# Performance work log

Measured on AMD Instinct MI355X. Metric: run time of the kernel, lower is better.

## Reference

```python
import jax, jax.numpy as jnp
import numpy as np

L, B, D_DEC, D_ALIGN, D_ENC = 2048, 64, 1024, 512, 1024


def setup_inputs() -> dict:
    key = jax.random.key(0)
    ks = jax.random.split(key, 8)
    s_tm1 = jax.random.normal(ks[0], (B, D_DEC), dtype=jnp.float32)
    xs_h = jax.random.normal(ks[1], (L, B, D_ENC), dtype=jnp.float32)
    uh = jax.random.normal(ks[2], (L, B, D_ALIGN), dtype=jnp.float32)
    # binary padding mask over source positions; guarantee >=1 valid position per column
    xs_mask = (jax.random.uniform(ks[3], (L, B)) > 0.1).astype(jnp.float32)
    xs_mask = xs_mask.at[0].set(1.0)
    sa_w = jax.random.normal(ks[4], (D_ALIGN, D_DEC), dtype=jnp.float32) / np.sqrt(D_DEC)
    sa_b = jnp.zeros((D_ALIGN,), dtype=jnp.float32)
    a1_w = jax.random.normal(ks[5], (1, D_ALIGN), dtype=jnp.float32) / np.sqrt(D_ALIGN)
    a1_b = jnp.zeros((1,), dtype=jnp.float32)
    return {"s_tm1": s_tm1, "xs_h": xs_h, "uh": uh, "xs_mask": xs_mask,
            "sa_w": sa_w, "sa_b": sa_b, "a1_w": a1_w, "a1_b": a1_b}


def reference(s_tm1, xs_h, uh, xs_mask, sa_w, sa_b, a1_w, a1_b):
    # sa(s_tm1): (B, A)
    proj = s_tm1 @ sa_w.T + sa_b
    # broadcast add over source positions, tanh: (L, B, A)
    act = jnp.tanh(proj[None, :, :] + uh)
    # a1(...).squeeze(2): (L, B)
    score = jnp.einsum('lba,a->lb', act, a1_w[0]) + a1_b[0]
    # masked softmax over dim 0 (exp * mask, then normalize) as in MaskSoftmax
    e = jnp.exp(score - jnp.max(score, axis=0, keepdims=True)) * xs_mask
    e_ij = e / jnp.sum(e, axis=0, keepdims=True)
    # weighted sum of encoder states: (B, D_ENC)
    attend = jnp.einsum('lb,lbd->bd', e_ij, xs_h)
    return (e_ij, attend)
```

## Files before the change

kernel.cpp:

```cpp
#include <hip/hip_runtime.h>

#define L 2048
#define B 64
#define D_DEC 1024
#define D_ALIGN 512
#define D_ENC 1024
#define LSPLIT 32

using u32 = unsigned int;
using u16 = unsigned short;

__device__ __forceinline__ u16 f2bf(float f) {
    u32 u = __float_as_uint(f);
    u32 r = (u + 0x7fffu + ((u >> 16) & 1u)) >> 16;
    return (u16)r;
}
__device__ __forceinline__ float tanh_fast(float x) {
    float t = __expf(2.0f * x);
    return 1.0f - 2.0f * __builtin_amdgcn_rcpf(t + 1.0f);
}
__device__ __forceinline__ bool detect_bf(const void* xs_mask) {
    return ((const u32*)xs_mask)[0] == 0x3F803F80u;
}
__device__ __forceinline__ float ldv(const void* p, size_t i, bool bf) {
    if (bf) return __uint_as_float(((u32)((const u16*)p)[i]) << 16);
    return ((const float*)p)[i];
}

__global__ __launch_bounds__(256) void proj_kernel(const void* __restrict__ s_tm1,
                                                   const void* __restrict__ sa_w,
                                                   const void* __restrict__ c0,
                                                   const void* __restrict__ c1,
                                                   const void* __restrict__ xs_mask,
                                                   float* __restrict__ proj) {
    bool bf = detect_bf(xs_mask);
    u32 w0 = ((const u32*)c0)[0], w1 = ((const u32*)c1)[0];
    const void* sab = (w0 == 0u || w1 != 0u) ? c0 : c1;
    int b = blockIdx.x >> 3;
    int wid = threadIdx.x >> 6, lane = threadIdx.x & 63;
    int a0 = (blockIdx.x & 7) * 64 + wid * 16;
    size_t sb = (size_t)b * D_DEC + (size_t)lane * 16;
    float sreg[16];
    if (!bf) {
        const float4* s4 = (const float4*)((const float*)s_tm1 + sb);
#pragma unroll
        for (int m = 0; m < 4; ++m) {
            float4 v = s4[m];
            sreg[4*m] = v.x; sreg[4*m+1] = v.y; sreg[4*m+2] = v.z; sreg[4*m+3] = v.w;
        }
    } else {
#pragma unroll
        for (int m = 0; m < 16; ++m) sreg[m] = ldv(s_tm1, sb + m, bf);
    }
#pragma unroll 4
    for (int ai = 0; ai < 16; ++ai) {
        int a = a0 + ai;
        size_t wb = (size_t)a * D_DEC + (size_t)lane * 16;
        float acc = 0.f;
        if (!bf) {
            const float4* w4 = (const float4*)((const float*)sa_w + wb);
#pragma unroll
            for (int m = 0; m < 4; ++m) {
                float4 v = w4[m];
                acc += sreg[4*m] * v.x + sreg[4*m+1] * v.y
                     + sreg[4*m+2] * v.z + sreg[4*m+3] * v.w;
            }
        } else {
#pragma unroll
            for (int m = 0; m < 16; ++m) acc += sreg[m] * ldv(sa_w, wb + m, bf);
        }
#pragma unroll
        for (int off = 32; off; off >>= 1) acc += __shfl_xor(acc, off, 64);
        if (lane == 0) proj[b * D_ALIGN + a] = acc + ldv(sab, a, bf);
    }
}

__global__ __launch_bounds__(256) void score_kernel(const void* __restrict__ uh,
                                                    const void* __restrict__ c0,
                                                    const void* __restrict__ c1,
                                                    const void* __restrict__ a1_b,
                                                    const void* __restrict__ xs_mask,
                                                    const float* __restrict__ proj,
                                                    float* __restrict__ score_t) {
    bool bf = detect_bf(xs_mask);
    u32 w0 = ((const u32*)c0)[0], w1 = ((const u32*)c1)[0];
    const void* a1w = (w1 != 0u || w0 == 0u) ? c1 : c0;
    int wave = blockIdx.x * 4 + (threadIdx.x >> 6);
    int lane = threadIdx.x & 63;
    int b = wave & (B - 1);
    int lc = wave >> 6;
    float bias = ldv(a1_b, 0, bf);
    float s[8];
    if (!bf) {
        const float4* p4 = (const float4*)proj + (size_t)b * 128;
        const float4* w4 = (const float4*)a1w;
        float4 p[2], w[2];
#pragma unroll
        for (int j = 0; j < 2; ++j) { p[j] = p4[j * 64 + lane]; w[j] = w4[j * 64 + lane]; }
#pragma unroll
        for (int il = 0; il < 8; ++il) {
            int l = lc * 8 + il;
            const float4* u4 = (const float4*)uh + (size_t)(l * B + b) * 128;
            float v = 0.f;
#pragma unroll
            for (int j = 0; j < 2; ++j) {
                float4 u = u4[j * 64 + lane];
                v += tanh_fast(p[j].x + u.x) * w[j].x;
                v += tanh_fast(p[j].y + u.y) * w[j].y;
                v += tanh_fast(p[j].z + u.z) * w[j].z;
                v += tanh_fast(p[j].w + u.w) * w[j].w;
            }
            s[il] = v;
        }
    } else {
        float p[8], w[8];
#pragma unroll
        for (int j = 0; j < 8; ++j) {
            p[j] = proj[b * D_ALIGN + j * 64 + lane];
            w[j] = ldv(a1w, j * 64 + lane, bf);
        }
#pragma unroll
        for (int il = 0; il < 8; ++il) {
            int l = lc * 8 + il;
            size_t base = (size_t)(l * B + b) * D_ALIGN;
            float v = 0.f;
#pragma unroll
            for (int j = 0; j < 8; ++j)
                v += tanh_fast(p[j] + ldv(uh, base + j * 64 + lane, bf)) * w[j];
            s[il] = v;
        }
    }
#pragma unroll
    for (int il = 0; il < 8; ++il) {
        float v = s[il];
#pragma unroll
        for (int off = 32; off; off >>= 1) v += __shfl_xor(v, off, 64);
        s[il] = v;
    }
    if (lane == 0) {
#pragma unroll
        for (int il = 0; il < 8; ++il)
            score_t[(size_t)b * L + lc * 8 + il] = s[il] + bias;
    }
}

__global__ __launch_bounds__(256) void softmax_kernel(const void* __restrict__ xs_mask,
                                                      const float* __restrict__ score_t,
                                                      float* __restrict__ e_t,
                                                      void* __restrict__ out) {
    bool bf = detect_bf(xs_mask);
    int b = blockIdx.x;
    int tid = threadIdx.x;
    __shared__ float red[256];
    float s[8];
    float mx = -1e30f;
#pragma unroll
    for (int i = 0; i < 8; ++i) {
        s[i] = score_t[(size_t)b * L + tid + i * 256];
        mx = fmaxf(mx, s[i]);
    }
    red[tid] = mx; __syncthreads();
    for (int off = 128; off; off >>= 1) {
        if (tid < off) red[tid] = fmaxf(red[tid], red[tid + off]);
        __syncthreads();
    }
    mx = red[0]; __syncthreads();
    float sum = 0.f;
#pragma unroll
    for (int i = 0; i < 8; ++i) {
        int l = tid + i * 256;
        s[i] = __expf(s[i] - mx) * ldv(xs_mask, (size_t)l * B + b, bf);
        sum += s[i];
    }
    red[tid] = sum; __syncthreads();
    for (int off = 128; off; off >>= 1) {
        if (tid < off) red[tid] += red[tid + off];
        __syncthreads();
    }
    float inv = 1.0f / red[0];
#pragma unroll
    for (int i = 0; i < 8; ++i) {
        int l = tid + i * 256;
        float e = s[i] * inv;
        e_t[(size_t)b * L + l] = e;
        if (bf) ((u16*)out)[(size_t)l * B + b] = f2bf(e);
        else    ((float*)out)[(size_t)l * B + b] = e;
    }
}

__global__ __launch_bounds__(256) void attend_kernel(const void* __restrict__ xs_h,
                                                     const void* __restrict__ xs_mask,
                                                     const float* __restrict__ e_t,
                                                     float* __restrict__ partial) {
    bool bf = detect_bf(xs_mask);
    int b = blockIdx.x & (B - 1);
    int ls = blockIdx.x >> 6;
    int tid = threadIdx.x;
    float ax = 0.f, ay = 0.f, az = 0.f, aw = 0.f;
    int lbeg = ls * (L / LSPLIT), lend = lbeg + (L / LSPLIT);
    if (!bf) {
        const float4* x4 = (const float4*)xs_h;
#pragma unroll 4
        for (int l = lbeg; l < lend; ++l) {
            float wgt = e_t[(size_t)b * L + l];
            float4 x = x4[(size_t)(l * B + b) * 256 + tid];
            ax += wgt * x.x; ay += wgt * x.y; az += wgt * x.z; aw += wgt * x.w;
        }
    } else {
#pragma unroll 2
        for (int l = lbeg; l < lend; ++l) {
            float wgt = e_t[(size_t)b * L + l];
            size_t base = (size_t)(l * B + b) * D_ENC + (size_t)tid * 4;
            ax += wgt * ldv(xs_h, base + 0, bf);
            ay += wgt * ldv(xs_h, base + 1, bf);
            az += wgt * ldv(xs_h, base + 2, bf);
            aw += wgt * ldv(xs_h, base + 3, bf);
        }
    }
    float4 r; r.x = ax; r.y = ay; r.z = az; r.w = aw;
    ((float4*)partial)[(size_t)(ls * B + b) * 256 + tid] = r;
}

__global__ __launch_bounds__(256) void reduce_kernel(const float* __restrict__ partial,
                                                     const void* __restrict__ xs_mask,
                                                     void* __restrict__ out) {
    bool bf = detect_bf(xs_mask);
    int idx = blockIdx.x * 256 + threadIdx.x;
    const float4* p4 = (const float4*)partial;
    float ax = 0.f, ay = 0.f, az = 0.f, aw = 0.f;
#pragma unroll
    for (int ls = 0; ls < LSPLIT; ++ls) {
        float4 v = p4[(size_t)ls * (B * D_ENC / 4) + idx];
        ax += v.x; ay += v.y; az += v.z; aw += v.w;
    }
    if (bf) {
        u16* o = (u16*)out + (size_t)L * B + (size_t)idx * 4;
        o[0] = f2bf(ax); o[1] = f2bf(ay); o[2] = f2bf(az); o[3] = f2bf(aw);
    } else {
        float4 r; r.x = ax; r.y = ay; r.z = az; r.w = aw;
        ((float4*)((float*)out + (size_t)L * B))[idx] = r;
    }
}

extern "C" void kernel_launch(void* const* d_in, const int* in_sizes, int n_in,
                              void* d_out, int out_size, void* d_ws, size_t ws_size,
                              hipStream_t stream) {
    const void *s_tm1 = d_in[0], *xs_h = d_in[1], *uh = d_in[2], *xs_mask = d_in[3],
               *sa_w = d_in[4];
    const void *a1_b = d_in[7];
    const void *p512[2] = {d_in[5], d_in[6]};
    int n512 = 0;
    for (int i = 0; i < n_in; ++i) {
        switch (in_sizes[i]) {
            case 134217728: xs_h = d_in[i]; break;
            case 67108864:  uh = d_in[i]; break;
            case 131072:    xs_mask = d_in[i]; break;
            case 65536:     s_tm1 = d_in[i]; break;
            case 524288:    sa_w = d_in[i]; break;
            case 1:         a1_b = d_in[i]; break;
            case 512:       if (n512 < 2) p512[n512] = d_in[i]; ++n512; break;
            default: break;
        }
    }
    const void* c0 = p512[0];
    const void* c1 = p512[1];

    float* proj    = (float*)d_ws;
    float* score_t = proj + 32768;
    float* e_t     = score_t + (size_t)L * B;
    float* partial = e_t + (size_t)L * B;

    proj_kernel<<<512, 256, 0, stream>>>(s_tm1, sa_w, c0, c1, xs_mask, proj);
    score_kernel<<<4096, 256, 0, stream>>>(uh, c0, c1, a1_b, xs_mask, proj, score_t);
    softmax_kernel<<<B, 256, 0, stream>>>(xs_mask, score_t, e_t, d_out);
    attend_kernel<<<LSPLIT * B, 256, 0, stream>>>(xs_h, xs_mask, e_t, partial);
    reduce_kernel<<<64, 256, 0, stream>>>(partial, xs_mask, d_out);
}
```

Baseline: 873.2 us.

## Skip masked positions in score and attend kernels, use wave-shuffle softmax reductions

The score kernel now reads the padding mask first and skips the uh loads and tanh work for masked positions, writing a large negative score for them. The attend kernel loads weights as float4 and skips the xs_h row load when a weight is exactly zero. The softmax kernel replaces the shared-memory tree reductions with wave shuffles and switches to contiguous float4 score loads and stores. Skipping masked positions changes the max used in the softmax, but the masked terms are multiplied by zero anyway, so results should match. The branches add divergence-free per-wave conditionals, and roughly 10% of rows are skipped since the mask is random.

```diff
diff --git a/kernel.cpp b/kernel.cpp
--- a/kernel.cpp
+++ b/kernel.cpp
@@ -90,6 +90,10 @@
     int b = wave & (B - 1);
     int lc = wave >> 6;
     float bias = ldv(a1_b, 0, bf);
+    float mk[8];
+#pragma unroll
+    for (int il = 0; il < 8; ++il)
+        mk[il] = ldv(xs_mask, (size_t)(lc * 8 + il) * B + b, bf);
     float s[8];
     if (!bf) {
         const float4* p4 = (const float4*)proj + (size_t)b * 128;
@@ -99,16 +103,18 @@
         for (int j = 0; j < 2; ++j) { p[j] = p4[j * 64 + lane]; w[j] = w4[j * 64 + lane]; }
 #pragma unroll
         for (int il = 0; il < 8; ++il) {
-            int l = lc * 8 + il;
-            const float4* u4 = (const float4*)uh + (size_t)(l * B + b) * 128;
             float v = 0.f;
-#pragma unroll
-            for (int j = 0; j < 2; ++j) {
-                float4 u = u4[j * 64 + lane];
-                v += tanh_fast(p[j].x + u.x) * w[j].x;
-                v += tanh_fast(p[j].y + u.y) * w[j].y;
-                v += tanh_fast(p[j].z + u.z) * w[j].z;
-                v += tanh_fast(p[j].w + u.w) * w[j].w;
+            if (mk[il] != 0.f) {
+                int l = lc * 8 + il;
+                const float4* u4 = (const float4*)uh + (size_t)(l * B + b) * 128;
+#pragma unroll
+                for (int j = 0; j < 2; ++j) {
+                    float4 u = u4[j * 64 + lane];
+                    v += tanh_fast(p[j].x + u.x) * w[j].x;
+                    v += tanh_fast(p[j].y + u.y) * w[j].y;
+                    v += tanh_fast(p[j].z + u.z) * w[j].z;
+                    v += tanh_fast(p[j].w + u.w) * w[j].w;
+                }
             }
             s[il] = v;
         }
@@ -121,12 +127,14 @@
         }
 #pragma unroll
         for (int il = 0; il < 8; ++il) {
-            int l = lc * 8 + il;
-            size_t base = (size_t)(l * B + b) * D_ALIGN;
             float v = 0.f;
-#pragma unroll
-            for (int j = 0; j < 8; ++j)
-                v += tanh_fast(p[j] + ldv(uh, base + j * 64 + lane, bf)) * w[j];
+            if (mk[il] != 0.f) {
+                int l = lc * 8 + il;
+                size_t base = (size_t)(l * B + b) * D_ALIGN;
+#pragma unroll
+                for (int j = 0; j < 8; ++j)
+                    v += tanh_fast(p[j] + ldv(uh, base + j * 64 + lane, bf)) * w[j];
+            }
             s[il] = v;
         }
     }
@@ -140,7 +148,8 @@
     if (lane == 0) {
 #pragma unroll
         for (int il = 0; il < 8; ++il)
-            score_t[(size_t)b * L + lc * 8 + il] = s[il] + bias;
+            score_t[(size_t)b * L + lc * 8 + il] =
+                (mk[il] != 0.f) ? s[il] + bias : -1e30f;
     }
 }
 
@@ -151,40 +160,46 @@
     bool bf = detect_bf(xs_mask);
     int b = blockIdx.x;
     int tid = threadIdx.x;
-    __shared__ float red[256];
-    float s[8];
+    int wid = tid >> 6, lane = tid & 63;
+    __shared__ float red[8];
+    const float4* sc4 = (const float4*)(score_t + (size_t)b * L);
+    float4 v0 = sc4[tid * 2], v1 = sc4[tid * 2 + 1];
+    float s[8] = {v0.x, v0.y, v0.z, v0.w, v1.x, v1.y, v1.z, v1.w};
+    float m[8];
+#pragma unroll
+    for (int j = 0; j < 8; ++j)
+        m[j] = ldv(xs_mask, (size_t)(tid * 8 + j) * B + b, bf);
     float mx = -1e30f;
 #pragma unroll
-    for (int i = 0; i < 8; ++i) {
-        s[i] = score_t[(size_t)b * L + tid + i * 256];
-        mx = fmaxf(mx, s[i]);
-    }
-    red[tid] = mx; __syncthreads();
-    for (int off = 128; off; off >>= 1) {
-        if (tid < off) red[tid] = fmaxf(red[tid], red[tid + off]);
-        __syncthreads();
-    }
-    mx = red[0]; __syncthreads();
+    for (int j = 0; j < 8; ++j) mx = fmaxf(mx, s[j]);
+#pragma unroll
+    for (int off = 32; off; off >>= 1) mx = fmaxf(mx, __shfl_xor(mx, off, 64));
+    if (lane == 0) red[wid] = mx;
+    __syncthreads();
+    mx = fmaxf(fmaxf(red[0], red[1]), fmaxf(red[2], red[3]));
     float sum = 0.f;
 #pragma unroll
-    for (int i = 0; i < 8; ++i) {
-        int l = tid + i * 256;
-        s[i] = __expf(s[i] - mx) * ldv(xs_mask, (size_t)l * B + b, bf);
-        sum += s[i];
-    }
-    red[tid] = sum; __syncthreads();
-    for (int off = 128; off; off >>= 1) {
-        if (tid < off) red[tid] += red[tid + off];
-        __syncthreads();
-    }
-    float inv = 1.0f / red[0];
-#pragma unroll
-    for (int i = 0; i < 8; ++i) {
-        int l = tid + i * 256;
-        float e = s[i] * inv;
-        e_t[(size_t)b * L + l] = e;
-        if (bf) ((u16*)out)[(size_t)l * B + b] = f2bf(e);
-        else    ((float*)out)[(size_t)l * B + b] = e;
+    for (int j = 0; j < 8; ++j) {
+        s[j] = __expf(s[j] - mx) * m[j];
+        sum += s[j];
+    }
+#pragma unroll
+    for (int off = 32; off; off >>= 1) sum += __shfl_xor(sum, off, 64);
+    if (lane == 0) red[4 + wid] = sum;
+    __syncthreads();
+    float inv = 1.0f / (red[4] + red[5] + red[6] + red[7]);
+#pragma unroll
+    for (int j = 0; j < 8; ++j) s[j] *= inv;
+    float4 e0, e1;
+    e0.x = s[0]; e0.y = s[1]; e0.z = s[2]; e0.w = s[3];
+    e1.x = s[4]; e1.y = s[5]; e1.z = s[6]; e1.w = s[7];
+    float4* et4 = (float4*)(e_t + (size_t)b * L);
+    et4[tid * 2] = e0; et4[tid * 2 + 1] = e1;
+#pragma unroll
+    for (int j = 0; j < 8; ++j) {
+        size_t o = (size_t)(tid * 8 + j) * B + b;
+        if (bf) ((u16*)out)[o] = f2bf(s[j]);
+        else    ((float*)out)[o] = s[j];
     }
 }
 
@@ -197,24 +212,47 @@
     int ls = blockIdx.x >> 6;
     int tid = threadIdx.x;
     float ax = 0.f, ay = 0.f, az = 0.f, aw = 0.f;
-    int lbeg = ls * (L / LSPLIT), lend = lbeg + (L / LSPLIT);
+    int lbeg = ls * (L / LSPLIT);
+    const float4* e4 = (const float4*)(e_t + (size_t)b * L) + (lbeg >> 2);
     if (!bf) {
         const float4* x4 = (const float4*)xs_h;
-#pragma unroll 4
-        for (int l = lbeg; l < lend; ++l) {
-            float wgt = e_t[(size_t)b * L + l];
-            float4 x = x4[(size_t)(l * B + b) * 256 + tid];
-            ax += wgt * x.x; ay += wgt * x.y; az += wgt * x.z; aw += wgt * x.w;
+#pragma unroll 2
+        for (int i = 0; i < (L / LSPLIT) / 4; ++i) {
+            float4 w = e4[i];
+            int l = lbeg + i * 4;
+            if (w.x != 0.f) {
+                float4 x = x4[(size_t)((l + 0) * B + b) * 256 + tid];
+                ax += w.x * x.x; ay += w.x * x.y; az += w.x * x.z; aw += w.x * x.w;
+            }
+            if (w.y != 0.f) {
+                float4 x = x4[(size_t)((l + 1) * B + b) * 256 + tid];
+                ax += w.y * x.x; ay += w.y * x.y; az += w.y * x.z; aw += w.y * x.w;
+            }
+            if (w.z != 0.f) {
+                float4 x = x4[(size_t)((l + 2) * B + b) * 256 + tid];
+                ax += w.z * x.x; ay += w.z * x.y; az += w.z * x.z; aw += w.z * x.w;
+            }
+            if (w.w != 0.f) {
+                float4 x = x4[(size_t)((l + 3) * B + b) * 256 + tid];
+                ax += w.w * x.x; ay += w.w * x.y; az += w.w * x.z; aw += w.w * x.w;
+            }
         }
     } else {
 #pragma unroll 2
-        for (int l = lbeg; l < lend; ++l) {
-            float wgt = e_t[(size_t)b * L + l];
-            size_t base = (size_t)(l * B + b) * D_ENC + (size_t)tid * 4;
-            ax += wgt * ldv(xs_h, base + 0, bf);
-            ay += wgt * ldv(xs_h, base + 1, bf);
-            az += wgt * ldv(xs_h, base + 2, bf);
-            aw += wgt * ldv(xs_h, base + 3, bf);
+        for (int i = 0; i < (L / LSPLIT) / 4; ++i) {
+            float4 w = e4[i];
+            float wv[4] = {w.x, w.y, w.z, w.w};
+#pragma unroll
+            for (int j = 0; j < 4; ++j) {
+                if (wv[j] != 0.f) {
+                    int l = lbeg + i * 4 + j;
+                    size_t base = (size_t)(l * B + b) * D_ENC + (size_t)tid * 4;
+                    ax += wv[j] * ldv(xs_h, base + 0, bf);
+                    ay += wv[j] * ldv(xs_h, base + 1, bf);
+                    az += wv[j] * ldv(xs_h, base + 2, bf);
+                    aw += wv[j] * ldv(xs_h, base + 3, bf);
+                }
+            }
         }
     }
     float4 r; r.x = ax; r.y = ay; r.z = az; r.w = aw;
```

After: 855.1 us. -2.1%, faster.
